# Optimization experiments

Hardware: AMD Instinct MI355X
Metric: run time of the kernel (lower is better)

## Reference

```python
import jax, jax.numpy as jnp
import numpy as np
import math

DIM = 1280
NUM_HEADS = 16
HEAD_DIM = DIM // NUM_HEADS  # 80
SEQ = 3072


def setup_inputs() -> dict:
    key = jax.random.key(0)
    ks = jax.random.split(key, 6)
    hidden_states = jax.random.normal(ks[0], (SEQ, DIM), dtype=jnp.float32)
    cu_seqlens = jnp.array([0, 768, 1536, 2304, 3072], dtype=jnp.int32)
    # rotary angles for half the head dim, as produced by the vision rotary embedding
    rotary_pos_emb = jax.random.uniform(ks[1], (SEQ, HEAD_DIM // 2), dtype=jnp.float32) * 10.0
    qkv_w = jax.random.normal(ks[2], (3 * DIM, DIM), dtype=jnp.float32) * (1.0 / math.sqrt(DIM))
    qkv_b = jax.random.normal(ks[3], (3 * DIM,), dtype=jnp.float32) * 0.02
    proj_w = jax.random.normal(ks[4], (DIM, DIM), dtype=jnp.float32) * (1.0 / math.sqrt(DIM))
    proj_b = jax.random.normal(ks[5], (DIM,), dtype=jnp.float32) * 0.02
    return {"hidden_states": hidden_states, "cu_seqlens": cu_seqlens,
            "rotary_pos_emb": rotary_pos_emb, "qkv_w": qkv_w, "qkv_b": qkv_b,
            "proj_w": proj_w, "proj_b": proj_b}


def _rotate_half(x):
    half = x.shape[-1] // 2
    return jnp.concatenate([-x[..., half:], x[..., :half]], axis=-1)


def _apply_rotary(t, rotary_pos_emb):
    # t: [seq, heads, head_dim]; rotary_pos_emb: [seq, head_dim//2]
    emb = jnp.concatenate([rotary_pos_emb, rotary_pos_emb], axis=-1)  # [seq, head_dim]
    cos = jnp.cos(emb)[:, None, :]
    sin = jnp.sin(emb)[:, None, :]
    return t * cos + _rotate_half(t) * sin


def reference(hidden_states, cu_seqlens, rotary_pos_emb, qkv_w, qkv_b, proj_w, proj_b):
    seq = hidden_states.shape[0]
    qkv = hidden_states @ qkv_w.T + qkv_b                       # [seq, 3*dim]
    qkv = qkv.reshape(seq, 3, NUM_HEADS, HEAD_DIM)
    q, k, v = qkv[:, 0], qkv[:, 1], qkv[:, 2]                   # [seq, h, d]
    q = _apply_rotary(q, rotary_pos_emb)
    k = _apply_rotary(k, rotary_pos_emb)

    # block-diagonal mask: token i attends to token j iff same segment
    seg = jnp.searchsorted(cu_seqlens[1:], jnp.arange(seq), side='right')
    same = seg[:, None] == seg[None, :]                         # [seq, seq] bool
    neg = jnp.finfo(q.dtype).min
    add_mask = jnp.where(same, jnp.float32(0), neg).astype(q.dtype)

    scale = 1.0 / math.sqrt(HEAD_DIM)
    scores = jnp.einsum('nhd,mhd->hnm', q, k) * scale           # [h, seq, seq]
    scores = scores + add_mask[None, :, :]
    attn = jax.nn.softmax(scores.astype(jnp.float32), axis=-1).astype(q.dtype)
    out = jnp.einsum('hnm,mhd->nhd', attn, v).reshape(seq, DIM)
    return out @ proj_w.T + proj_b
```

## Files before the change

### kernel.cpp

```cpp
#include <hip/hip_runtime.h>

#define SEQ 3072
#define NH 16
#define HD 80
#define SEGLEN 768

typedef unsigned short u16;
typedef unsigned int u32;
typedef float f32x4 __attribute__((ext_vector_type(4)));
typedef __bf16 bf16x8 __attribute__((ext_vector_type(8)));
typedef short short8 __attribute__((ext_vector_type(8)));
typedef u16 u16x4 __attribute__((ext_vector_type(4)));

#define WAITV(N) asm volatile("s_waitcnt vmcnt(" #N ")" ::: "memory")

__device__ __forceinline__ u16 f2bf(float f) {
  u32 u = __builtin_bit_cast(u32, f);
  u32 r = u + 0x7fffu + ((u >> 16) & 1u);
  return (u16)(r >> 16);
}
__device__ __forceinline__ float bf2f(u16 x) {
  u32 u = ((u32)x) << 16;
  return __builtin_bit_cast(float, u);
}

__device__ __forceinline__ f32x4 mfma16(short8 a, short8 b, f32x4 c) {
  return __builtin_amdgcn_mfma_f32_16x16x32_bf16(
      __builtin_bit_cast(bf16x8, a), __builtin_bit_cast(bf16x8, b), c, 0, 0, 0);
}

__device__ __forceinline__ void gload_lds16(const u16* g, u16* l) {
  __builtin_amdgcn_global_load_lds(
      (const __attribute__((address_space(1))) u32*)(g),
      (__attribute__((address_space(3))) u32*)(l), 16, 0, 0);
}

__global__ __launch_bounds__(256) void cvt3(const float* __restrict__ a, u16* __restrict__ ao, int na,
                                            const float* __restrict__ b, u16* __restrict__ bo, int nb,
                                            const float* __restrict__ c, u16* __restrict__ co, int nc) {
  int i = blockIdx.x * 256 + threadIdx.x;
  const float* src;
  u16* dst;
  int n;
  if (i < na) { src = a; dst = ao; n = i; }
  else if (i < na + nb) { src = b; dst = bo; n = i - na; }
  else if (i < na + nb + nc) { src = c; dst = co; n = i - na - nb; }
  else return;
  f32x4 v = ((const f32x4*)src)[n];
  u16x4 o;
  o[0] = f2bf(v[0]); o[1] = f2bf(v[1]); o[2] = f2bf(v[2]); o[3] = f2bf(v[3]);
  ((u16x4*)dst)[n] = o;
}

template <int OUT_BF16, int WM, int WN>
__global__ __launch_bounds__(256) void gemm_p3(
    const u16* __restrict__ A, const u16* __restrict__ B,
    const float* __restrict__ bias, void* __restrict__ Cv,
    int M, int N, int K) {
  constexpr int BM = 32 * WM, BN = 32 * WN;
  constexpr int ROWS = BM + BN;
  constexpr int L = ROWS / 64;
  __shared__ u16 LB[3][ROWS * 32];
  const int tid = threadIdx.x, lane = tid & 63, w = tid >> 6;
  const int wr = (w >> 1) * (WM * 16), wc = (w & 1) * (WN * 16);
  const int lr = lane & 15, lg = lane >> 4;
  const int gy = gridDim.y;
  const int fc = blockIdx.x * gy + blockIdx.y;
  const int cpx = (gridDim.x * gy) >> 3;
  const int f = (fc & 7) * cpx + (fc >> 3);
  const int bx = f / gy, by = f % gy;
  const int br = by * BM, bc = bx * BN;
  const int NT = K >> 5;

  f32x4 acc[WM][WN];
#pragma unroll
  for (int m = 0; m < WM; ++m)
#pragma unroll
    for (int n = 0; n < WN; ++n) acc[m][n] = (f32x4){0.f, 0.f, 0.f, 0.f};

  const u16* sp[L];
#pragma unroll
  for (int c = 0; c < L; ++c) {
    int ch = c * 256 + tid;
    int row = ch >> 2, sl = ch & 3;
    int scol = ((sl - (row >> 1)) & 3) << 3;
    sp[c] = (row < BM ? A + (br + row) * (size_t)K
                      : B + (bc + row - BM) * (size_t)K) + scol;
  }
  auto stage = [&](int t, int buf) {
#pragma unroll
    for (int c = 0; c < L; ++c)
      gload_lds16(sp[c] + t * 32, &LB[buf][(c * 256 + tid) * 8]);
  };

  int aoff[WM], boff[WN];
#pragma unroll
  for (int m = 0; m < WM; ++m) {
    int row = wr + m * 16 + lr;
    aoff[m] = row * 64 + ((lg + (row >> 1)) & 3) * 16;
  }
#pragma unroll
  for (int n = 0; n < WN; ++n) {
    int row = BM + wc + n * 16 + lr;
    boff[n] = row * 64 + ((lg + (row >> 1)) & 3) * 16;
  }

  auto step = [&](int t, int buf, bool issue, int wn) {
    if (issue) stage(t + 2, (t + 2) % 3);
    const char* base = (const char*)&LB[buf][0];
    short8 af[WM], bf[WN];
#pragma unroll
    for (int m = 0; m < WM; ++m) af[m] = *(const short8*)(base + aoff[m]);
#pragma unroll
    for (int n = 0; n < WN; ++n) bf[n] = *(const short8*)(base + boff[n]);
#pragma unroll
    for (int m = 0; m < WM; ++m)
#pragma unroll
      for (int n = 0; n < WN; ++n) acc[m][n] = mfma16(af[m], bf[n], acc[m][n]);
    if (wn == 4) WAITV(4);
    else if (wn == 3) WAITV(3);
    else if (wn == 0) WAITV(0);
    if (wn >= 0) __builtin_amdgcn_s_barrier();
  };

  stage(0, 0);
  stage(1, 1);
  if constexpr (L == 4) WAITV(4);
  else WAITV(3);
  __builtin_amdgcn_s_barrier();

  int t = 0;
  for (; t + 3 <= NT - 2; t += 3) {
    step(t + 0, 0, true, L);
    step(t + 1, 1, true, L);
    step(t + 2, 2, true, L);
  }
  step(NT - 4, 0, true, L);
  step(NT - 3, 1, true, L);
  step(NT - 2, 2, false, 0);
  step(NT - 1, 0, false, -1);

#pragma unroll
  for (int n = 0; n < WN; ++n) {
    int col = bc + wc + n * 16 + lr;
    float bv = bias[col];
#pragma unroll
    for (int m = 0; m < WM; ++m) {
      int rowb = br + wr + m * 16 + lg * 4;
#pragma unroll
      for (int r = 0; r < 4; ++r) {
        float v = acc[m][n][r] + bv;
        if (OUT_BF16)
          ((u16*)Cv)[(rowb + r) * N + col] = f2bf(v);
        else
          ((float*)Cv)[(rowb + r) * N + col] = v;
      }
    }
  }
}

__global__ __launch_bounds__(256) void prep_kern(
    const u16* __restrict__ qkvb, const float* __restrict__ rpe,
    u16* __restrict__ qb, u16* __restrict__ kb, u16* __restrict__ vt) {
  const int bid = blockIdx.x, tid = threadIdx.x;
  if (bid < 3072) {
    const float QSCL = 0.16129841769519493f;
    const u16* row = qkvb + bid * 3840;
#pragma unroll
    for (int it = 0; it < 5; ++it) {
      int idx = it * 256 + tid;
      int d = idx % 80;
      float e = rpe[bid * 40 + (d % 40)];
      float s, c;
      sincosf(e, &s, &c);
      float qv = bf2f(row[idx]);
      float qo = (d < 40) ? -bf2f(row[idx + 40]) : bf2f(row[idx - 40]);
      float kv = bf2f(row[1280 + idx]);
      float ko = (d < 40) ? -bf2f(row[1280 + idx + 40]) : bf2f(row[1280 + idx - 40]);
      int o = bid * 1280 + idx;
      qb[o] = f2bf((qv * c + qo * s) * QSCL);
      kb[o] = f2bf(kv * c + ko * s);
    }
  } else {
    __shared__ u16 tile[64 * 84];
    const int vb = bid - 3072;
    const int s0 = (vb % 48) * 64, h = vb / 48;
#pragma unroll
    for (int c = 0; c < 20; ++c) {
      int ch = c * 256 + tid;
      int r = ch / 80, d = ch % 80;
      tile[r * 84 + d] = qkvb[(s0 + r) * 3840 + 2560 + h * 80 + d];
    }
    __syncthreads();
#pragma unroll
    for (int c = 0; c < 20; ++c) {
      int ch = c * 256 + tid;
      int d = ch >> 6, r = ch & 63;
      vt[(h * 96 + d) * 3072 + s0 + r] = tile[r * 84 + d];
    }
    if (tid < 64) vt[(h * 96 + 80) * 3072 + s0 + tid] = 0x3F80;
  }
}

__global__ __launch_bounds__(256) void attn_kern(
    const u16* __restrict__ qb, const u16* __restrict__ kb,
    const u16* __restrict__ vt, u16* __restrict__ ob) {
  __shared__ u16 SH[26176];
  char* shb = (char*)SH;
  const int tid = threadIdx.x, lane = tid & 63, w = tid >> 6;
  const int lr = lane & 15, lg = lane >> 4;
  const int xcd = blockIdx.x & 7, t = blockIdx.x >> 3;
  const int qt = t % 12, shhi = t / 12;
  const int sh = xcd + shhi * 8;
  const int seg = sh >> 4, h = sh & 15;
  const int qrow = seg * SEGLEN + qt * 64 + w * 16 + lr;

  short8 qf[3];
#pragma unroll
  for (int kk = 0; kk < 3; ++kk) {
    int d = kk * 32 + lg * 8;
    if (d < 80)
      qf[kk] = *(const short8*)(qb + qrow * 1280 + h * 80 + d);
    else
      qf[kk] = (short8){0, 0, 0, 0, 0, 0, 0, 0};
  }
  f32x4 oa[6];
#pragma unroll
  for (int n = 0; n < 6; ++n) oa[n] = (f32x4){0.f, 0.f, 0.f, 0.f};
  float mrow[4] = {-1e30f, -1e30f, -1e30f, -1e30f};

  const u16* kseg = kb + seg * SEGLEN * 1280 + h * 80;
  const u16* vseg = vt + (h * 96) * 3072 + seg * SEGLEN;

  auto stageK = [&](int buf, int it) {
    const u16* kbase = kseg + it * 64 * 1280;
#pragma unroll
    for (int c = 0; c < 4; ++c) {
      int ch = c * 256 + tid;
      int kv = ch >> 4, sl = ch & 15;
      gload_lds16(kbase + kv * 1280 + ((sl ^ (kv & 7)) << 3),
                  (u16*)(shb + buf * 16384 + ch * 16));
    }
  };
  auto stageV = [&](int it) {
    const u16* vbase = vseg + it * 64;
#pragma unroll
    for (int c = 0; c < 3; ++c) {
      int ch = c * 256 + tid;
      if (ch < 648) {
        int d = ch >> 3, sl = ch & 7;
        gload_lds16(vbase + d * 3072 + ((sl ^ (d & 7)) << 3),
                    (u16*)(shb + 32768 + ch * 16));
      }
    }
  };

  stageK(0, 0);
  stageV(0);
  __syncthreads();
  int cur = 0;
  char* PsW = shb + 43136 + w * 2304;
  const char* Vc = shb + 32768;

  for (int it = 0; it < 12; ++it) {
    if (it > 0) stageV(it);
    if (it < 11) stageK(cur ^ 1, it + 1);
    const char* Kc = shb + cur * 16384;
    f32x4 sf[4];
#pragma unroll
    for (int n = 0; n < 4; ++n) {
      sf[n] = (f32x4){0.f, 0.f, 0.f, 0.f};
#pragma unroll
      for (int kk = 0; kk < 3; ++kk) {
        int row = n * 16 + lr;
        int X = kk * 64 + lg * 16;
        short8 kf = *(const short8*)(Kc + row * 256 + (X ^ ((row & 7) << 4)));
        __builtin_amdgcn_s_setprio(1);
        sf[n] = mfma16(qf[kk], kf, sf[n]);
        __builtin_amdgcn_s_setprio(0);
      }
    }
    float mx[4];
#pragma unroll
    for (int r = 0; r < 4; ++r) {
      float a = fmaxf(fmaxf(sf[0][r], sf[1][r]), fmaxf(sf[2][r], sf[3][r]));
      a = fmaxf(a, __shfl_xor(a, 1, 16));
      a = fmaxf(a, __shfl_xor(a, 2, 16));
      a = fmaxf(a, __shfl_xor(a, 4, 16));
      a = fmaxf(a, __shfl_xor(a, 8, 16));
      mx[r] = a;
    }
    float need = fmaxf(fmaxf(mx[0] - mrow[0], mx[1] - mrow[1]),
                       fmaxf(mx[2] - mrow[2], mx[3] - mrow[3]));
    if (!__all(need <= 8.0f)) {
#pragma unroll
      for (int r = 0; r < 4; ++r) {
        float m = fmaxf(mrow[r], mx[r]);
        float f = exp2f(mrow[r] - m);
        mrow[r] = m;
#pragma unroll
        for (int n = 0; n < 6; ++n) oa[n][r] *= f;
      }
    }
#pragma unroll
    for (int r = 0; r < 4; ++r) {
      float p0 = exp2f(sf[0][r] - mrow[r]), p1 = exp2f(sf[1][r] - mrow[r]);
      float p2 = exp2f(sf[2][r] - mrow[r]), p3 = exp2f(sf[3][r] - mrow[r]);
      int offb = (lg * 4 + r) * 144 + lr * 2;
      *(u16*)(PsW + offb + ((lg ^ 0) << 5)) = f2bf(p0);
      *(u16*)(PsW + offb + ((lg ^ 1) << 5)) = f2bf(p1);
      *(u16*)(PsW + offb + ((lg ^ 2) << 5)) = f2bf(p2);
      *(u16*)(PsW + offb + ((lg ^ 3) << 5)) = f2bf(p3);
    }
    __syncthreads();
#pragma unroll
    for (int kt = 0; kt < 2; ++kt) {
      short8 pf = *(const short8*)(PsW + lr * 144 +
                                   ((((kt << 1) + (lg >> 1)) ^ (lr >> 2)) << 5) +
                                   ((lg & 1) << 4));
#pragma unroll
      for (int n = 0; n < 6; ++n) {
        int dcol = n * 16 + lr;
        int X = kt * 64 + lg * 16;
        short8 vf = *(const short8*)(Vc + dcol * 128 + (X ^ ((dcol & 7) << 4)));
        __builtin_amdgcn_s_setprio(1);
        oa[n] = mfma16(pf, vf, oa[n]);
        __builtin_amdgcn_s_setprio(0);
      }
    }
    __syncthreads();
    cur ^= 1;
  }
#pragma unroll
  for (int r = 0; r < 4; ++r) {
    float lsum = __shfl(oa[5][r], lane & 48, 64);
    float linv = 1.0f / lsum;
    int orow = seg * SEGLEN + qt * 64 + w * 16 + lg * 4 + r;
#pragma unroll
    for (int n = 0; n < 5; ++n)
      ob[orow * 1280 + h * 80 + n * 16 + lr] = f2bf(oa[n][r] * linv);
  }
}

extern "C" void kernel_launch(void* const* d_in, const int* in_sizes, int n_in,
                              void* d_out, int out_size, void* d_ws, size_t ws_size,
                              hipStream_t stream) {
  const float* hs = (const float*)d_in[0];
  const float* rpe = (const float*)d_in[2];
  const float* qkvw = (const float*)d_in[3];
  const float* qkv_b = (const float*)d_in[4];
  const float* pw = (const float*)d_in[5];
  const float* pb = (const float*)d_in[6];
  float* out = (float*)d_out;

  char* ws = (char*)d_ws;
  u16* hsb = (u16*)(ws);
  u16* wqkvb = (u16*)(ws + 7864320);
  u16* wprojb = (u16*)(ws + 17694720);
  u16* qkvb = (u16*)(ws + 20971520);
  u16* vt = (u16*)(ws + 44564480);
  u16* qb = hsb;
  u16* kb = wqkvb;
  u16* aob = qkvb;

  cvt3<<<10240, 256, 0, stream>>>(hs, hsb, 983040, qkvw, wqkvb, 1228800, pw, wprojb, 409600);
  gemm_p3<1, 4, 4><<<dim3(30, 24), 256, 0, stream>>>(hsb, wqkvb, qkv_b, qkvb, 3072, 3840, 1280);
  prep_kern<<<3840, 256, 0, stream>>>(qkvb, rpe, qb, kb, vt);
  attn_kern<<<768, 256, 0, stream>>>(qb, kb, vt, aob);
  gemm_p3<0, 2, 4><<<dim3(10, 48), 256, 0, stream>>>(aob, wprojb, pb, out, 3072, 1280, 1280);
}
```

Measured before the change: 135.4 us.

## Generalize GEMM to configurable wave grid and use 512-thread 256x128 QKV tile

Templates the pipelined bf16 GEMM on waves per M/N so block size and tile shape are configurable, and launches the QKV projection with 8 waves and a 256x128 tile, halving the block count. The goal is more reuse per LDS load and fewer redundant global reads. It also removes the XCD-aware block index swizzle, which may reduce L2 locality. The larger tile raises LDS use per block and gives fewer, larger blocks on the grid.

```diff
diff --git a/kernel.cpp b/kernel.cpp
--- a/kernel.cpp
+++ b/kernel.cpp
@@ -52,24 +52,21 @@
   ((u16x4*)dst)[n] = o;
 }
 
-template <int OUT_BF16, int WM, int WN>
-__global__ __launch_bounds__(256) void gemm_p3(
+template <int OUT_BF16, int WM, int WN, int WAVES_M, int WAVES_N>
+__global__ __launch_bounds__(WAVES_M * WAVES_N * 64) void gemm_pw(
     const u16* __restrict__ A, const u16* __restrict__ B,
     const float* __restrict__ bias, void* __restrict__ Cv,
     int M, int N, int K) {
-  constexpr int BM = 32 * WM, BN = 32 * WN;
+  constexpr int BM = WAVES_M * WM * 16, BN = WAVES_N * WN * 16;
+  constexpr int THREADS = WAVES_M * WAVES_N * 64;
   constexpr int ROWS = BM + BN;
-  constexpr int L = ROWS / 64;
+  constexpr int L = (ROWS * 4) / THREADS;
+  static_assert(L == 3, "pipeline tuned for L=3");
   __shared__ u16 LB[3][ROWS * 32];
   const int tid = threadIdx.x, lane = tid & 63, w = tid >> 6;
-  const int wr = (w >> 1) * (WM * 16), wc = (w & 1) * (WN * 16);
+  const int wr = (w / WAVES_N) * (WM * 16), wc = (w % WAVES_N) * (WN * 16);
   const int lr = lane & 15, lg = lane >> 4;
-  const int gy = gridDim.y;
-  const int fc = blockIdx.x * gy + blockIdx.y;
-  const int cpx = (gridDim.x * gy) >> 3;
-  const int f = (fc & 7) * cpx + (fc >> 3);
-  const int bx = f / gy, by = f % gy;
-  const int br = by * BM, bc = bx * BN;
+  const int br = blockIdx.y * BM, bc = blockIdx.x * BN;
   const int NT = K >> 5;
 
   f32x4 acc[WM][WN];
@@ -81,7 +78,7 @@
   const u16* sp[L];
 #pragma unroll
   for (int c = 0; c < L; ++c) {
-    int ch = c * 256 + tid;
+    int ch = c * THREADS + tid;
     int row = ch >> 2, sl = ch & 3;
     int scol = ((sl - (row >> 1)) & 3) << 3;
     sp[c] = (row < BM ? A + (br + row) * (size_t)K
@@ -90,7 +87,7 @@
   auto stage = [&](int t, int buf) {
 #pragma unroll
     for (int c = 0; c < L; ++c)
-      gload_lds16(sp[c] + t * 32, &LB[buf][(c * 256 + tid) * 8]);
+      gload_lds16(sp[c] + t * 32, &LB[buf][(c * THREADS + tid) * 8]);
   };
 
   int aoff[WM], boff[WN];
@@ -117,26 +114,24 @@
     for (int m = 0; m < WM; ++m)
 #pragma unroll
       for (int n = 0; n < WN; ++n) acc[m][n] = mfma16(af[m], bf[n], acc[m][n]);
-    if (wn == 4) WAITV(4);
-    else if (wn == 3) WAITV(3);
+    if (wn == 3) WAITV(3);
     else if (wn == 0) WAITV(0);
     if (wn >= 0) __builtin_amdgcn_s_barrier();
   };
 
   stage(0, 0);
   stage(1, 1);
-  if constexpr (L == 4) WAITV(4);
-  else WAITV(3);
+  WAITV(3);
   __builtin_amdgcn_s_barrier();
 
   int t = 0;
   for (; t + 3 <= NT - 2; t += 3) {
-    step(t + 0, 0, true, L);
-    step(t + 1, 1, true, L);
-    step(t + 2, 2, true, L);
-  }
-  step(NT - 4, 0, true, L);
-  step(NT - 3, 1, true, L);
+    step(t + 0, 0, true, 3);
+    step(t + 1, 1, true, 3);
+    step(t + 2, 2, true, 3);
+  }
+  step(NT - 4, 0, true, 3);
+  step(NT - 3, 1, true, 3);
   step(NT - 2, 2, false, 0);
   step(NT - 1, 0, false, -1);
 
@@ -364,8 +359,8 @@
   u16* aob = qkvb;
 
   cvt3<<<10240, 256, 0, stream>>>(hs, hsb, 983040, qkvw, wqkvb, 1228800, pw, wprojb, 409600);
-  gemm_p3<1, 4, 4><<<dim3(30, 24), 256, 0, stream>>>(hsb, wqkvb, qkv_b, qkvb, 3072, 3840, 1280);
+  gemm_pw<1, 4, 4, 4, 2><<<dim3(30, 12), 512, 0, stream>>>(hsb, wqkvb, qkv_b, qkvb, 3072, 3840, 1280);
   prep_kern<<<3840, 256, 0, stream>>>(qkvb, rpe, qb, kb, vt);
   attn_kern<<<768, 256, 0, stream>>>(qb, kb, vt, aob);
-  gemm_p3<0, 2, 4><<<dim3(10, 48), 256, 0, stream>>>(aob, wprojb, pb, out, 3072, 1280, 1280);
-}
+  gemm_pw<0, 2, 4, 2, 2><<<dim3(10, 48), 256, 0, stream>>>(aob, wprojb, pb, out, 3072, 1280, 1280);
+}
```

After: 139.5 us. 3.0% more time.

## Replace QKV projection GEMM with 256x256-tile 8-wave double-buffered kernel

Applied to the files above, without the earlier changes.

Adds a new bf16 GEMM using 512 threads, 256x256 output tiles and K-steps of 64. Each K-step is split into four quarter phases that interleave global-to-LDS staging with MFMA work, and MFMA blocks are wrapped in setprio. It replaces the 128x128 gemm_p3 launch for the QKV projection, giving more reuse per LDS load. The trade-off is only 180 workgroups (fewer than the CU count) plus heavy register and LDS use per block. gemm_p3 is pinned to its L=3 configuration.

```diff
diff --git a/kernel.cpp b/kernel.cpp
--- a/kernel.cpp
+++ b/kernel.cpp
@@ -52,6 +52,106 @@
   ((u16x4*)dst)[n] = o;
 }
 
+__global__ __launch_bounds__(512) void gemm_8p(
+    const u16* __restrict__ A, const u16* __restrict__ B,
+    const float* __restrict__ bias, u16* __restrict__ C,
+    int M, int N, int K) {
+  __shared__ u16 LB[2 * 4 * 8192];
+  char* lds = (char*)LB;
+  const int tid = threadIdx.x, lane = tid & 63, w = tid >> 6;
+  const int wm = w >> 2, wn = w & 3;
+  const int lr = lane & 15, lg = lane >> 4;
+  const int br = blockIdx.y * 256, bc = blockIdx.x * 256;
+  const int NT = K >> 6;
+
+  f32x4 acc[8][4];
+#pragma unroll
+  for (int m = 0; m < 8; ++m)
+#pragma unroll
+    for (int n = 0; n < 4; ++n) acc[m][n] = (f32x4){0.f, 0.f, 0.f, 0.f};
+
+  const int r0 = tid >> 2, s0 = tid & 3;
+  const int r1 = r0 + 128;
+  const u16* sA0 = A + (br + r0) * (size_t)K + (((s0 - (r0 >> 1)) & 3) << 3);
+  const u16* sA1 = A + (br + r1) * (size_t)K + (((s0 - (r1 >> 1)) & 3) << 3);
+  const u16* sB0 = B + (bc + r0) * (size_t)K + (((s0 - (r0 >> 1)) & 3) << 3);
+  const u16* sB1 = B + (bc + r1) * (size_t)K + (((s0 - (r1 >> 1)) & 3) << 3);
+  const int d0 = tid * 16, d1 = (tid + 512) * 16;
+
+  auto stg = [&](const u16* g0, const u16* g1, int kcol, int buf, int half) {
+    char* hb = lds + buf * 65536 + half * 16384;
+    gload_lds16(g0 + kcol, (u16*)(hb + d0));
+    gload_lds16(g1 + kcol, (u16*)(hb + d1));
+  };
+
+  int aoff[8], boff[4];
+#pragma unroll
+  for (int m = 0; m < 8; ++m) {
+    int row = wm * 128 + m * 16 + lr;
+    aoff[m] = row * 64 + ((lg + (row >> 1)) & 3) * 16;
+  }
+#pragma unroll
+  for (int n = 0; n < 4; ++n) {
+    int row = wn * 64 + n * 16 + lr;
+    boff[n] = row * 64 + ((lg + (row >> 1)) & 3) * 16;
+  }
+
+  stg(sA0, sA1, 0, 0, 0);
+  stg(sA0, sA1, 32, 0, 1);
+  stg(sB0, sB1, 0, 0, 2);
+  stg(sB0, sB1, 32, 0, 3);
+  stg(sA0, sA1, 64, 1, 0);
+  stg(sB0, sB1, 64, 1, 2);
+  WAITV(4);
+  __builtin_amdgcn_s_barrier();
+
+  for (int t = 0; t < NT; ++t) {
+    const int p = t & 1;
+    const char* Ab = lds + p * 65536;
+    const char* Bb = Ab + 32768;
+#pragma unroll
+    for (int q = 0; q < 4; ++q) {
+      const char* Ah = Ab + (q >> 1) * 16384;
+      const char* Bh = Bb + (q >> 1) * 16384;
+      short8 af[8], bf0, bf1;
+#pragma unroll
+      for (int m = 0; m < 8; ++m) af[m] = *(const short8*)(Ah + aoff[m]);
+      const int nb = (q & 1) * 2;
+      bf0 = *(const short8*)(Bh + boff[nb]);
+      bf1 = *(const short8*)(Bh + boff[nb + 1]);
+      if (q == 0) { if (t + 1 < NT) stg(sA0, sA1, (t + 1) * 64 + 32, p ^ 1, 1); }
+      else if (q == 1) { if (t + 1 < NT) stg(sB0, sB1, (t + 1) * 64 + 32, p ^ 1, 3); }
+      else if (q == 2) { if (t + 2 < NT) stg(sA0, sA1, (t + 2) * 64, p, 0); }
+      else { if (t + 2 < NT) stg(sB0, sB1, (t + 2) * 64, p, 2); }
+      __builtin_amdgcn_s_setprio(1);
+#pragma unroll
+      for (int m = 0; m < 8; ++m) {
+        acc[m][nb] = mfma16(af[m], bf0, acc[m][nb]);
+        acc[m][nb + 1] = mfma16(af[m], bf1, acc[m][nb + 1]);
+      }
+      __builtin_amdgcn_s_setprio(0);
+      if (q == 3) {
+        if (t == NT - 2) WAITV(0);
+        else if (t < NT - 2) WAITV(4);
+      }
+      __builtin_amdgcn_s_barrier();
+    }
+  }
+
+#pragma unroll
+  for (int n = 0; n < 4; ++n) {
+    int col = bc + wn * 64 + n * 16 + lr;
+    float bv = bias[col];
+#pragma unroll
+    for (int m = 0; m < 8; ++m) {
+      int rowb = br + wm * 128 + m * 16 + lg * 4;
+#pragma unroll
+      for (int r = 0; r < 4; ++r)
+        C[(size_t)(rowb + r) * N + col] = f2bf(acc[m][n][r] + bv);
+    }
+  }
+}
+
 template <int OUT_BF16, int WM, int WN>
 __global__ __launch_bounds__(256) void gemm_p3(
     const u16* __restrict__ A, const u16* __restrict__ B,
@@ -60,6 +160,7 @@
   constexpr int BM = 32 * WM, BN = 32 * WN;
   constexpr int ROWS = BM + BN;
   constexpr int L = ROWS / 64;
+  static_assert(L == 3, "tuned for L=3");
   __shared__ u16 LB[3][ROWS * 32];
   const int tid = threadIdx.x, lane = tid & 63, w = tid >> 6;
   const int wr = (w >> 1) * (WM * 16), wc = (w & 1) * (WN * 16);
@@ -117,26 +218,24 @@
     for (int m = 0; m < WM; ++m)
 #pragma unroll
       for (int n = 0; n < WN; ++n) acc[m][n] = mfma16(af[m], bf[n], acc[m][n]);
-    if (wn == 4) WAITV(4);
-    else if (wn == 3) WAITV(3);
+    if (wn == 3) WAITV(3);
     else if (wn == 0) WAITV(0);
     if (wn >= 0) __builtin_amdgcn_s_barrier();
   };
 
   stage(0, 0);
   stage(1, 1);
-  if constexpr (L == 4) WAITV(4);
-  else WAITV(3);
+  WAITV(3);
   __builtin_amdgcn_s_barrier();
 
   int t = 0;
   for (; t + 3 <= NT - 2; t += 3) {
-    step(t + 0, 0, true, L);
-    step(t + 1, 1, true, L);
-    step(t + 2, 2, true, L);
-  }
-  step(NT - 4, 0, true, L);
-  step(NT - 3, 1, true, L);
+    step(t + 0, 0, true, 3);
+    step(t + 1, 1, true, 3);
+    step(t + 2, 2, true, 3);
+  }
+  step(NT - 4, 0, true, 3);
+  step(NT - 3, 1, true, 3);
   step(NT - 2, 2, false, 0);
   step(NT - 1, 0, false, -1);
 
@@ -364,7 +463,7 @@
   u16* aob = qkvb;
 
   cvt3<<<10240, 256, 0, stream>>>(hs, hsb, 983040, qkvw, wqkvb, 1228800, pw, wprojb, 409600);
-  gemm_p3<1, 4, 4><<<dim3(30, 24), 256, 0, stream>>>(hsb, wqkvb, qkv_b, qkvb, 3072, 3840, 1280);
+  gemm_8p<<<dim3(15, 12), 512, 0, stream>>>(hsb, wqkvb, qkv_b, qkvb, 3072, 3840, 1280);
   prep_kern<<<3840, 256, 0, stream>>>(qkvb, rpe, qb, kb, vt);
   attn_kern<<<768, 256, 0, stream>>>(qb, kb, vt, aob);
   gemm_p3<0, 2, 4><<<dim3(10, 48), 256, 0, stream>>>(aob, wprojb, pb, out, 3072, 1280, 1280);
```

New measurement: 132.0 us. 2.5% less time.
